# Performance work log

Measured on AMD Instinct MI355X. Metric: run time of the kernel, lower is better.

## Reference

```python
import jax, jax.numpy as jnp
import numpy as np
from jax import lax

K_SIZE = 7
STRIDES = (2, 2, 2, 3)

def causal_conv_block(x, w, b, stride):
    # x: (B, Cin, L); w: (Cout, Cin, K); left-pad K-1 for causality
    xp = jnp.pad(x, ((0, 0), (0, 0), (K_SIZE - 1, 0)))
    y = lax.conv_general_dilated(xp, w, window_strides=(stride,), padding='VALID',
                                 dimension_numbers=('NCH', 'OIH', 'NCH'))
    return jax.nn.elu(y + b[None, :, None])

def vq_indices(z, codebook):
    # z: (B, D, T); codebook: (K, D) -> indices (B, T)
    zt = jnp.transpose(z, (0, 2, 1))                      # (B, T, D)
    d = (jnp.sum(zt * zt, axis=-1, keepdims=True)
         - 2.0 * jnp.einsum('btd,kd->btk', zt, codebook)
         + jnp.sum(codebook * codebook, axis=-1)[None, None, :])  # (B, T, K)
    return jnp.argmin(d, axis=-1)

def setup_inputs() -> dict:
    key = jax.random.key(0)
    ks = jax.random.split(key, 16)
    B, L = 64, 48000
    chans = [1, 16, 32, 64, 64]  # in->out schedule from min(64, 16*2**i)
    inp = {'x': jax.random.normal(ks[0], (B, 1, L), dtype=jnp.float32)}
    for i in range(4):
        cin, cout = chans[i], chans[i + 1]
        scale = 1.0 / np.sqrt(cin * K_SIZE)
        inp[f'w{i}'] = jax.random.normal(ks[1 + 2 * i], (cout, cin, K_SIZE), jnp.float32) * scale
        inp[f'b{i}'] = jax.random.normal(ks[2 + 2 * i], (cout,), jnp.float32) * 0.01
    # pre_quant: 64 -> LATENT_DIM*NUM_CODEBOOKS = 128
    inp['wq'] = jax.random.normal(ks[10], (128, 64, K_SIZE), jnp.float32) * (1.0 / np.sqrt(64 * K_SIZE))
    inp['bq'] = jax.random.normal(ks[11], (128,), jnp.float32) * 0.01
    inp['codebooks'] = jax.random.normal(ks[12], (2, 1024, 64), jnp.float32)  # (num_cb, K, D)
    return inp

def reference(x, w0, b0, w1, b1, w2, b2, w3, b3, wq, bq, codebooks):
    h = x
    for w, b, s in ((w0, b0, STRIDES[0]), (w1, b1, STRIDES[1]),
                    (w2, b2, STRIDES[2]), (w3, b3, STRIDES[3])):
        h = causal_conv_block(h, w, b, s)
    z_e = causal_conv_block(h, wq, bq, 1)           # (B, 128, T)
    z0, z1 = jnp.split(z_e, 2, axis=1)              # chunk along channel dim
    idx0 = vq_indices(z0, codebooks[0])             # (B, T) int
    idx1 = vq_indices(z1, codebooks[1])
    return jnp.stack([idx0, idx1], axis=0)          # (num_cb, B, T)
```

## Files before the change

kernel.cpp:

```cpp
#include <hip/hip_runtime.h>
#include <hip/hip_bf16.h>
#include <cstddef>


using bf16x8 = __attribute__((ext_vector_type(8))) short;
using s16x4  = __attribute__((ext_vector_type(4))) short;
using f32x4  = __attribute__((ext_vector_type(4))) float;

static __device__ __forceinline__ short f2bf(float f) {
    __hip_bfloat16 h = __float2bfloat16(f);
    union { __hip_bfloat16 h; short s; } u; u.h = h;
    return u.s;
}
static __device__ __forceinline__ float bf2f(short s) {
    union { unsigned u; float f; } v;
    v.u = ((unsigned)(unsigned short)s) << 16;
    return v.f;
}
static __device__ __forceinline__ void split3(float v, short& s0, short& s1, short& s2) {
    s0 = f2bf(v);  float r1 = v  - bf2f(s0);
    s1 = f2bf(r1); float r2 = r1 - bf2f(s1);
    s2 = f2bf(r2);
}
static __device__ __forceinline__ float elu(float v) {
    return v > 0.0f ? v : expm1f(v);
}

__global__ __launch_bounds__(256) void conv0_kernel(
    const float* __restrict__ x, const float* __restrict__ w,
    const float* __restrict__ bias, float* __restrict__ H0)
{
    __shared__ float xs[261];
    int tb = blockIdx.x, b = blockIdx.y;
    int t0 = tb * 128;
    int tid = threadIdx.x, lane = tid & 63;
    int wv = __builtin_amdgcn_readfirstlane(tid >> 6);

    const float* xb = x + (size_t)b * 48000;
    int g0 = t0 * 2 - 6;
    for (int i = tid; i < 261; i += 256) {
        int gx = g0 + i;
        xs[i] = (gx >= 0 && gx < 48000) ? xb[gx] : 0.0f;
    }
    __syncthreads();

    int co0 = wv * 4;
    float acc[4][2];
    #pragma unroll
    for (int c = 0; c < 4; ++c) { acc[c][0] = 0.f; acc[c][1] = 0.f; }

    float xw[2][7];
    #pragma unroll
    for (int u = 0; u < 2; ++u)
        #pragma unroll
        for (int k = 0; k < 7; ++k)
            xw[u][k] = xs[(lane + 64 * u) * 2 + k];
    #pragma unroll
    for (int c = 0; c < 4; ++c) {
        const float* wp = w + (size_t)(co0 + c) * 7;
        #pragma unroll
        for (int k = 0; k < 7; ++k) {
            float wk = wp[k];
            acc[c][0] = fmaf(wk, xw[0][k], acc[c][0]);
            acc[c][1] = fmaf(wk, xw[1][k], acc[c][1]);
        }
    }

    #pragma unroll
    for (int u = 0; u < 2; ++u) {
        int t = t0 + lane + 64 * u;
        if (t < 24000) {
            float4 vv;
            vv.x = elu(acc[0][u] + bias[co0 + 0]);
            vv.y = elu(acc[1][u] + bias[co0 + 1]);
            vv.z = elu(acc[2][u] + bias[co0 + 2]);
            vv.w = elu(acc[3][u] + bias[co0 + 3]);
            *(float4*)(H0 + ((size_t)b * 12000 + (t >> 1)) * 32 + (t & 1) * 16 + co0) = vv;
        }
    }
}

template<int CIN, int COUT, int TAPS>
__global__ void wprep3_kernel(const float* __restrict__ w, short* __restrict__ frag)
{
    constexpr int KC = CIN / 32;
    int co = threadIdx.x;
    if (co >= COUT) return;
    int mt = co >> 4, nc = co & 15;
    for (int kc = 0; kc < KC; ++kc)
        for (int k = 0; k < TAPS; ++k)
            #pragma unroll
            for (int lh = 0; lh < 4; ++lh) {
                bf16x8 p0, p1, p2;
                #pragma unroll
                for (int j = 0; j < 8; ++j) {
                    int ci = kc * 32 + lh * 8 + j;
                    float f = w[(size_t)co * CIN * 7 + ci * 7 + k];
                    short a, bb, c; split3(f, a, bb, c);
                    p0[j] = a; p1[j] = bb; p2[j] = c;
                }
                size_t base = ((size_t)(mt * KC + kc) * TAPS + k) * 3;
                int off = (lh * 16 + nc) * 8;
                *(bf16x8*)(frag + (base + 0) * 512 + off) = p0;
                *(bf16x8*)(frag + (base + 1) * 512 + off) = p1;
                *(bf16x8*)(frag + (base + 2) * 512 + off) = p2;
            }
}

template<int CINH, int COUT>
__global__ void wprep3_ps_kernel(const float* __restrict__ w, short* __restrict__ frag)
{
    constexpr int CIN = 2 * CINH;
    constexpr int KC  = CIN / 32;
    int co = threadIdx.x;
    if (co >= COUT) return;
    int mt = co >> 4, nc = co & 15;
    for (int kc = 0; kc < KC; ++kc)
        for (int m = 0; m < 4; ++m)
            #pragma unroll
            for (int lh = 0; lh < 4; ++lh) {
                bf16x8 p0, p1, p2;
                #pragma unroll
                for (int j = 0; j < 8; ++j) {
                    int cp = kc * 32 + lh * 8 + j;
                    float f;
                    if (cp < CINH)  f = w[(size_t)co * CINH * 7 + cp * 7 + 2 * m];
                    else if (m < 3) f = w[(size_t)co * CINH * 7 + (cp - CINH) * 7 + 2 * m + 1];
                    else            f = 0.0f;
                    short a, bb, c; split3(f, a, bb, c);
                    p0[j] = a; p1[j] = bb; p2[j] = c;
                }
                size_t base = ((size_t)(mt * KC + kc) * 4 + m) * 3;
                int off = (lh * 16 + nc) * 8;
                *(bf16x8*)(frag + (base + 0) * 512 + off) = p0;
                *(bf16x8*)(frag + (base + 1) * 512 + off) = p1;
                *(bf16x8*)(frag + (base + 2) * 512 + off) = p2;
            }
}

template<int S, int CIN, int COUT, int NTL, int TAPS, int PAD, int OUTMODE>
__global__ __launch_bounds__(256) void conv_mfma3_kernel(
    const float* __restrict__ Hin, const short* __restrict__ wfrag,
    const float* __restrict__ bias, float* __restrict__ Hout,
    int Lin, int Lout)
{
    constexpr int KC   = CIN / 32;
    constexpr int MT   = COUT / 16;
    constexpr int NT   = NTL * 64;
    constexpr int ROWS = (NT - 1) * S + TAPS;
    constexpr int ROWB = CIN * 2;
    constexpr int NSL  = CIN / 4;
    __shared__ __align__(16) short pl0[ROWS * CIN];
    __shared__ __align__(16) short pl1[ROWS * CIN];
    __shared__ __align__(16) short pl2[ROWS * CIN];

    int nb = blockIdx.x, b = blockIdx.y;
    int t0 = nb * NT;
    int tid = threadIdx.x, lane = tid & 63, wv = tid >> 6;
    int g0 = t0 * S - PAD;

    const float* inb = Hin + (size_t)b * Lin * CIN;
    for (int e = tid; e < ROWS * NSL; e += 256) {
        int rr = e / NSL, sl = e % NSL;
        int g = g0 + rr;
        float4 v = {0.f, 0.f, 0.f, 0.f};
        if (g >= 0 && g < Lin)
            v = *(const float4*)(inb + (size_t)g * CIN + sl * 4);
        int xr = (CIN == 64) ? (rr & 7) : ((rr >> 1) & 3);
        int byte = rr * ROWB + ((((sl >> 1) ^ xr) << 4) | ((sl & 1) << 3));
        s16x4 q0, q1, q2;
        short a0, a1, a2;
        split3(v.x, a0, a1, a2); q0[0] = a0; q1[0] = a1; q2[0] = a2;
        split3(v.y, a0, a1, a2); q0[1] = a0; q1[1] = a1; q2[1] = a2;
        split3(v.z, a0, a1, a2); q0[2] = a0; q1[2] = a1; q2[2] = a2;
        split3(v.w, a0, a1, a2); q0[3] = a0; q1[3] = a1; q2[3] = a2;
        *(s16x4*)((char*)pl0 + byte) = q0;
        *(s16x4*)((char*)pl1 + byte) = q1;
        *(s16x4*)((char*)pl2 + byte) = q2;
    }
    __syncthreads();

    f32x4 acc[NTL][MT];
    #pragma unroll
    for (int n = 0; n < NTL; ++n)
        #pragma unroll
        for (int m = 0; m < MT; ++m) acc[n][m] = (f32x4){0.f, 0.f, 0.f, 0.f};

    int ncol = lane & 15, nq = lane >> 4;

    for (int k = 0; k < TAPS; ++k) {
        #pragma unroll
        for (int kc = 0; kc < KC; ++kc) {
            int colb = (kc * 32 + nq * 8) * 2;
            bf16x8 B0[NTL], B1[NTL], B2[NTL];
            #pragma unroll
            for (int ntl = 0; ntl < NTL; ++ntl) {
                int r  = S * ((wv * NTL + ntl) * 16 + ncol) + k;
                int xr = (CIN == 64) ? (r & 7) : ((r >> 1) & 3);
                int byte = r * ROWB + (colb ^ (xr << 4));
                B0[ntl] = *(const bf16x8*)((char*)pl0 + byte);
                B1[ntl] = *(const bf16x8*)((char*)pl1 + byte);
                B2[ntl] = *(const bf16x8*)((char*)pl2 + byte);
            }
            #pragma unroll
            for (int m = 0; m < MT; ++m) {
                size_t base = ((size_t)(m * KC + kc) * TAPS + k) * 3;
                bf16x8 a0 = *(const bf16x8*)(wfrag + (base + 0) * 512 + lane * 8);
                bf16x8 a1 = *(const bf16x8*)(wfrag + (base + 1) * 512 + lane * 8);
                bf16x8 a2 = *(const bf16x8*)(wfrag + (base + 2) * 512 + lane * 8);
                #pragma unroll
                for (int ntl = 0; ntl < NTL; ++ntl) {
                    f32x4 a = acc[ntl][m];
                    a = __builtin_amdgcn_mfma_f32_16x16x32_bf16(a0, B0[ntl], a, 0, 0, 0);
                    a = __builtin_amdgcn_mfma_f32_16x16x32_bf16(a1, B0[ntl], a, 0, 0, 0);
                    a = __builtin_amdgcn_mfma_f32_16x16x32_bf16(a2, B0[ntl], a, 0, 0, 0);
                    a = __builtin_amdgcn_mfma_f32_16x16x32_bf16(a0, B1[ntl], a, 0, 0, 0);
                    a = __builtin_amdgcn_mfma_f32_16x16x32_bf16(a1, B1[ntl], a, 0, 0, 0);
                    a = __builtin_amdgcn_mfma_f32_16x16x32_bf16(a0, B2[ntl], a, 0, 0, 0);
                    acc[ntl][m] = a;
                }
            }
        }
    }

    #pragma unroll
    for (int ntl = 0; ntl < NTL; ++ntl) {
        int n = t0 + (wv * NTL + ntl) * 16 + ncol;
        if (n < Lout) {
            #pragma unroll
            for (int m = 0; m < MT; ++m) {
                int co0 = m * 16 + nq * 4;
                float4 bb = *(const float4*)(bias + co0);
                float4 vv;
                vv.x = elu(acc[ntl][m][0] + bb.x);
                vv.y = elu(acc[ntl][m][1] + bb.y);
                vv.z = elu(acc[ntl][m][2] + bb.z);
                vv.w = elu(acc[ntl][m][3] + bb.w);
                if constexpr (OUTMODE == 0) {
                    *(float4*)(Hout + ((size_t)b * Lout + n) * COUT + co0) = vv;
                } else if constexpr (OUTMODE == 1) {
                    *(float4*)(Hout + ((size_t)b * (Lout >> 1) + (n >> 1)) * (2 * COUT)
                               + (n & 1) * COUT + co0) = vv;
                } else {
                    Hout[((size_t)b * COUT + co0 + 0) * Lout + n] = vv.x;
                    Hout[((size_t)b * COUT + co0 + 1) * Lout + n] = vv.y;
                    Hout[((size_t)b * COUT + co0 + 2) * Lout + n] = vv.z;
                    Hout[((size_t)b * COUT + co0 + 3) * Lout + n] = vv.w;
                }
            }
        }
    }
}

__global__ __launch_bounds__(256) void vq_prep_kernel(
    const float* __restrict__ cbs, float* __restrict__ cc, short* __restrict__ cbf)
{
    int c = blockIdx.x * 256 + threadIdx.x;
    if (c >= 2048) return;
    int cb = c >> 10, nl = c & 1023;
    const float* row = cbs + (size_t)c * 64;
    float v[64];
    float s = 0.f;
    #pragma unroll
    for (int i = 0; i < 16; ++i) {
        float4 q = ((const float4*)row)[i];
        v[4*i+0] = q.x; v[4*i+1] = q.y; v[4*i+2] = q.z; v[4*i+3] = q.w;
        s += q.x*q.x + q.y*q.y + q.z*q.z + q.w*q.w;
    }
    cc[c] = s;
    int nt = nl >> 4, nc = nl & 15;
    #pragma unroll
    for (int kc = 0; kc < 2; ++kc)
        #pragma unroll
        for (int lh = 0; lh < 4; ++lh) {
            bf16x8 ph, pl;
            #pragma unroll
            for (int j = 0; j < 8; ++j) {
                float f = -2.0f * v[kc*32 + lh*8 + j];
                short h = f2bf(f);
                ph[j] = h;
                pl[j] = f2bf(f - bf2f(h));
            }
            size_t base = ((((size_t)cb*64 + nt)*2 + kc)*2);
            *(bf16x8*)(cbf + ((base + 0)*64 + (lh*16 + nc)) * 8) = ph;
            *(bf16x8*)(cbf + ((base + 1)*64 + (lh*16 + nc)) * 8) = pl;
        }
}

__global__ void zero_cnt_kernel(int* cnt) {
    if (threadIdx.x == 0 && blockIdx.x == 0) { cnt[0] = 0; cnt[1] = 0; }
}

#define VQ_MARGIN 0.04f

__global__ __launch_bounds__(256) void vq_mfma_kernel(
    const float* __restrict__ z, const short* __restrict__ cbf,
    const float* __restrict__ ccg, int* __restrict__ out,
    int* __restrict__ cnt, int* __restrict__ list0, int* __restrict__ list1)
{
    __shared__ short zf[2][8*2*64*8];
    __shared__ short cbc[8*2*2*64*8];

    const int T = 2000;
    int mblk = blockIdx.x;
    int cb   = blockIdx.y;
    int b    = blockIdx.z;
    int t0   = mblk * 128;
    int tid  = threadIdx.x;
    int lane = tid & 63;
    int wv   = tid >> 6;
    int* list = cb ? list1 : list0;

    const float* zb = z + ((size_t)b*128 + (size_t)cb*64) * T;
    for (int e = tid; e < 128 * 8; e += 256) {
        int tl = e & 127;
        int d0 = (e >> 7) * 8;
        int tt = t0 + tl; if (tt > T - 1) tt = T - 1;
        bf16x8 hi, lo;
        #pragma unroll
        for (int jj = 0; jj < 8; ++jj) {
            float v = zb[(size_t)(d0 + jj) * T + tt];
            short h = f2bf(v);
            hi[jj] = h;
            lo[jj] = f2bf(v - bf2f(h));
        }
        int mt = tl >> 4, kc = d0 >> 5;
        int lw = ((d0 & 31) >> 3) * 16 + (tl & 15);
        int idx = ((mt*2 + kc)*64 + lw) * 8;
        *(bf16x8*)&zf[0][idx] = hi;
        *(bf16x8*)&zf[1][idx] = lo;
    }
    __syncthreads();

    bf16x8 ah[2][2], al[2][2];
    #pragma unroll
    for (int mtl = 0; mtl < 2; ++mtl)
        #pragma unroll
        for (int kc = 0; kc < 2; ++kc) {
            int idx = ((((wv*2+mtl)*2 + kc)*64) + lane)*8;
            ah[mtl][kc] = *(const bf16x8*)&zf[0][idx];
            al[mtl][kc] = *(const bf16x8*)&zf[1][idx];
        }

    float best[2][4], second[2][4]; int bidx[2][4];
    #pragma unroll
    for (int m = 0; m < 2; ++m)
        #pragma unroll
        for (int j = 0; j < 4; ++j) { best[m][j] = 3.4e38f; second[m][j] = 3.4e38f; bidx[m][j] = 0; }

    const short* cbase = cbf + (size_t)cb * (64*2*2*64*8);
    const float* ccb   = ccg + cb * 1024;
    int c15 = lane & 15;

    for (int ch = 0; ch < 8; ++ch) {
        __syncthreads();
        {
            const float4* src = (const float4*)(cbase + (size_t)ch * (8*2*2*64*8));
            float4* dst = (float4*)cbc;
            #pragma unroll
            for (int i = 0; i < 8; ++i) dst[tid + 256*i] = src[tid + 256*i];
        }
        __syncthreads();

        #pragma unroll
        for (int ntl = 0; ntl < 8; ++ntl) {
            bf16x8 b0h = *(const bf16x8*)&cbc[(((ntl*2 + 0)*2 + 0)*64 + lane)*8];
            bf16x8 b0l = *(const bf16x8*)&cbc[(((ntl*2 + 0)*2 + 1)*64 + lane)*8];
            bf16x8 b1h = *(const bf16x8*)&cbc[(((ntl*2 + 1)*2 + 0)*64 + lane)*8];
            bf16x8 b1l = *(const bf16x8*)&cbc[(((ntl*2 + 1)*2 + 1)*64 + lane)*8];
            int  code = ch*128 + ntl*16 + c15;
            float ccv = ccb[code];
            #pragma unroll
            for (int mtl = 0; mtl < 2; ++mtl) {
                f32x4 p = {ccv, ccv, ccv, ccv};
                p = __builtin_amdgcn_mfma_f32_16x16x32_bf16(ah[mtl][0], b0h, p, 0, 0, 0);
                p = __builtin_amdgcn_mfma_f32_16x16x32_bf16(al[mtl][0], b0h, p, 0, 0, 0);
                p = __builtin_amdgcn_mfma_f32_16x16x32_bf16(ah[mtl][0], b0l, p, 0, 0, 0);
                p = __builtin_amdgcn_mfma_f32_16x16x32_bf16(ah[mtl][1], b1h, p, 0, 0, 0);
                p = __builtin_amdgcn_mfma_f32_16x16x32_bf16(al[mtl][1], b1h, p, 0, 0, 0);
                p = __builtin_amdgcn_mfma_f32_16x16x32_bf16(ah[mtl][1], b1l, p, 0, 0, 0);
                #pragma unroll
                for (int j = 0; j < 4; ++j) {
                    float s = p[j];
                    bool lt = s < best[mtl][j];
                    second[mtl][j] = __builtin_amdgcn_fmed3f(best[mtl][j], s, second[mtl][j]);
                    best[mtl][j]   = fminf(best[mtl][j], s);
                    bidx[mtl][j]   = lt ? code : bidx[mtl][j];
                }
            }
        }
    }

    #pragma unroll
    for (int m = 0; m < 2; ++m)
        #pragma unroll
        for (int j = 0; j < 4; ++j) {
            float bv = best[m][j], sv = second[m][j]; int bi = bidx[m][j];
            #pragma unroll
            for (int d = 1; d < 16; d <<= 1) {
                float ob = __shfl_xor(bv, d, 64);
                float os = __shfl_xor(sv, d, 64);
                int   oi = __shfl_xor(bi, d, 64);
                float loser = fmaxf(bv, ob);
                sv = fminf(fminf(sv, os), loser);
                bool sw = ob < bv;
                bv = fminf(bv, ob);
                bi = sw ? oi : bi;
            }
            if ((lane & 15) == 0) {
                int t = t0 + (wv*2 + m)*16 + (lane >> 4)*4 + j;
                if (t < T) {
                    out[((size_t)cb*64 + b)*T + t] = bi;
                    if (sv - bv < VQ_MARGIN) {
                        int pos = atomicAdd(&cnt[cb], 1);
                        list[pos] = (b << 11) | t;
                    }
                }
            }
        }
}

__global__ __launch_bounds__(256) void vq_rescore_kernel(
    const float* __restrict__ H3, const float* __restrict__ wq,
    const float* __restrict__ bq, const float* __restrict__ cbs,
    const float* __restrict__ ccg, const int* __restrict__ cnt,
    const int* __restrict__ list0, const int* __restrict__ list1,
    int* __restrict__ out)
{
    const int T = 2000;
    __shared__ float hp[4][2][448];
    __shared__ float zsh[4][2][64];
    int tid = threadIdx.x, lane = tid & 63, wv = tid >> 6;
    int cb = blockIdx.y;
    const int* list = cb ? list1 : list0;
    int count = cnt[cb];
    int gw = blockIdx.x * 4 + wv, nw = gridDim.x * 4;

    const float* cbase = cbs + (size_t)cb * 1024 * 64;
    const float* ccb   = ccg + cb * 1024;
    int d = cb * 64 + lane;
    const float4* wp = (const float4*)(wq + (size_t)d * 448);
    float bqd = bq[d];

    for (int i0 = gw * 2; i0 < count; i0 += nw * 2) {
        int e0 = list[i0];
        int e1 = (i0 + 1 < count) ? list[i0 + 1] : e0;
        int b0 = e0 >> 11, t0 = e0 & 2047;
        int b1 = e1 >> 11, t1 = e1 & 2047;

        size_t base0 = (size_t)b0 * T * 64;
        size_t base1 = (size_t)b1 * T * 64;
        #pragma unroll
        for (int kk = 0; kk < 7; ++kk) {
            int a0 = t0 - 6 + kk, a1 = t1 - 6 + kk;
            hp[wv][0][lane * 7 + kk] = (a0 >= 0) ? H3[base0 + (size_t)a0 * 64 + lane] : 0.0f;
            hp[wv][1][lane * 7 + kk] = (a1 >= 0) ? H3[base1 + (size_t)a1 * 64 + lane] : 0.0f;
        }

        float p00=0.f,p01=0.f,p02=0.f,p03=0.f, p10=0.f,p11=0.f,p12=0.f,p13=0.f;
        #pragma unroll 8
        for (int q = 0; q < 112; ++q) {
            float4 w4 = wp[q];
            float4 h0 = *(const float4*)&hp[wv][0][4 * q];
            float4 h1 = *(const float4*)&hp[wv][1][4 * q];
            p00 = fmaf(w4.x, h0.x, p00); p01 = fmaf(w4.y, h0.y, p01);
            p02 = fmaf(w4.z, h0.z, p02); p03 = fmaf(w4.w, h0.w, p03);
            p10 = fmaf(w4.x, h1.x, p10); p11 = fmaf(w4.y, h1.y, p11);
            p12 = fmaf(w4.z, h1.z, p12); p13 = fmaf(w4.w, h1.w, p13);
        }
        float z0 = (p00 + p01) + (p02 + p03) + bqd; z0 = z0 > 0.f ? z0 : expm1f(z0);
        float z1 = (p10 + p11) + (p12 + p13) + bqd; z1 = z1 > 0.f ? z1 : expm1f(z1);
        zsh[wv][0][lane] = z0;
        zsh[wv][1][lane] = z1;

        float bv0 = 3.4e38f, bv1 = 3.4e38f; int bi0 = 0, bi1 = 0;
        for (int ii = 0; ii < 16; ++ii) {
            int code = ii * 64 + lane;
            const float4* cp = (const float4*)(cbase + (size_t)code * 64);
            float d00=0.f,d01=0.f,d02=0.f,d03=0.f, d10=0.f,d11=0.f,d12=0.f,d13=0.f;
            #pragma unroll
            for (int q = 0; q < 16; ++q) {
                float4 cv = cp[q];
                float4 za = *(const float4*)&zsh[wv][0][4 * q];
                float4 zc = *(const float4*)&zsh[wv][1][4 * q];
                d00 = fmaf(za.x, cv.x, d00); d01 = fmaf(za.y, cv.y, d01);
                d02 = fmaf(za.z, cv.z, d02); d03 = fmaf(za.w, cv.w, d03);
                d10 = fmaf(zc.x, cv.x, d10); d11 = fmaf(zc.y, cv.y, d11);
                d12 = fmaf(zc.z, cv.z, d12); d13 = fmaf(zc.w, cv.w, d13);
            }
            float cc0 = ccb[code];
            float s0 = fmaf(-2.0f, (d00 + d01) + (d02 + d03), cc0);
            float s1 = fmaf(-2.0f, (d10 + d11) + (d12 + d13), cc0);
            if (s0 < bv0) { bv0 = s0; bi0 = code; }
            if (s1 < bv1) { bv1 = s1; bi1 = code; }
        }
        #pragma unroll
        for (int dd = 1; dd < 64; dd <<= 1) {
            float ov0 = __shfl_xor(bv0, dd, 64); int oi0 = __shfl_xor(bi0, dd, 64);
            if (ov0 < bv0 || (ov0 == bv0 && oi0 < bi0)) { bv0 = ov0; bi0 = oi0; }
            float ov1 = __shfl_xor(bv1, dd, 64); int oi1 = __shfl_xor(bi1, dd, 64);
            if (ov1 < bv1 || (ov1 == bv1 && oi1 < bi1)) { bv1 = ov1; bi1 = oi1; }
        }
        if (lane == 0) {
            out[((size_t)cb * 64 + b0) * T + t0] = bi0;
            out[((size_t)cb * 64 + b1) * T + t1] = bi1;
        }
    }
}

extern "C" void kernel_launch(void* const* d_in, const int* in_sizes, int n_in,
                              void* d_out, int out_size, void* d_ws, size_t ws_size,
                              hipStream_t stream)
{
    const float* x   = (const float*)d_in[0];
    const float* w0  = (const float*)d_in[1];
    const float* b0  = (const float*)d_in[2];
    const float* w1  = (const float*)d_in[3];
    const float* b1  = (const float*)d_in[4];
    const float* w2  = (const float*)d_in[5];
    const float* b2  = (const float*)d_in[6];
    const float* w3  = (const float*)d_in[7];
    const float* b3  = (const float*)d_in[8];
    const float* wq  = (const float*)d_in[9];
    const float* bq  = (const float*)d_in[10];
    const float* cbs = (const float*)d_in[11];
    int* out = (int*)d_out;

    char* r1 = (char*)d_ws;
    char* r2 = r1 + 98304000;
    float* H0 = (float*)r1;
    float* H1 = (float*)r2;
    float* H2 = (float*)r1;
    float* H3 = (float*)r2;
    float* z  = (float*)(r2 + 32768000);

    short* wf1 = (short*)d_out;
    short* wf2 = wf1 + 12288;
    short* wf3 = wf1 + 61440;
    short* wf4 = wf1 + 147456;

    short* cbf   = (short*)r1;
    float* cc    = (float*)(r1 + 524288);
    int*   cnt   = (int*)(r1 + 540000);
    int*   list0 = (int*)(r1 + 1000000);
    int*   list1 = (int*)(r1 + 2100000);

    wprep3_ps_kernel<16, 32><<<1, 32, 0, stream>>>(w1, wf1);
    wprep3_ps_kernel<32, 64><<<1, 64, 0, stream>>>(w2, wf2);
    wprep3_kernel<64, 64, 7><<<1, 64, 0, stream>>>(w3, wf3);
    wprep3_kernel<64, 128, 7><<<1, 128, 0, stream>>>(wq, wf4);

    conv0_kernel<<<dim3(188, 64), 256, 0, stream>>>(x, w0, b0, H0);
    conv_mfma3_kernel<1, 32, 32, 2, 4, 3, 1><<<dim3(94, 64), 256, 0, stream>>>(
        H0, wf1, b1, H1, 12000, 12000);
    conv_mfma3_kernel<1, 64, 64, 2, 4, 3, 0><<<dim3(47, 64), 256, 0, stream>>>(
        H1, wf2, b2, H2, 6000, 6000);
    conv_mfma3_kernel<3, 64, 64, 1, 7, 6, 0><<<dim3(32, 64), 256, 0, stream>>>(
        H2, wf3, b3, H3, 6000, 2000);

    vq_prep_kernel<<<8, 256, 0, stream>>>(cbs, cc, cbf);
    zero_cnt_kernel<<<1, 64, 0, stream>>>(cnt);

    conv_mfma3_kernel<1, 64, 128, 2, 7, 6, 2><<<dim3(16, 64), 256, 0, stream>>>(
        H3, wf4, bq, z, 2000, 2000);

    vq_mfma_kernel<<<dim3(16, 2, 64), 256, 0, stream>>>(z, cbf, cc, out, cnt, list0, list1);
    vq_rescore_kernel<<<dim3(512, 2), 256, 0, stream>>>(H3, wq, bq, cbs, cc, cnt, list0, list1, out);
}
```

Baseline: 726.9 us.

## Prefetch next codebook chunk into registers and alias shared buffers in VQ kernel

Changes the VQ MFMA kernel to load the next codebook chunk from global memory into registers while the current chunk is being processed, so the global fetch overlaps compute. The z fragment buffers and the codebook staging buffer now alias one shared array, reducing LDS per block so more blocks may fit per CU. It also raises wave priority around the MFMA sequence. The cost is higher register pressure from holding the prefetched data, which may lower occupancy.

After: 763.8 us. +5.1%, slower.

```diff
diff --git a/kernel.cpp b/kernel.cpp
--- a/kernel.cpp
+++ b/kernel.cpp
@@ -298,8 +298,10 @@
     const float* __restrict__ ccg, int* __restrict__ out,
     int* __restrict__ cnt, int* __restrict__ list0, int* __restrict__ list1)
 {
-    __shared__ short zf[2][8*2*64*8];
-    __shared__ short cbc[8*2*2*64*8];
+    __shared__ __align__(16) short sbuf[16384];
+    short* zf0 = sbuf;
+    short* zf1 = sbuf + 8192;
+    short* cbc = sbuf;
 
     const int T = 2000;
     int mblk = blockIdx.x;
@@ -327,8 +329,8 @@
         int mt = tl >> 4, kc = d0 >> 5;
         int lw = ((d0 & 31) >> 3) * 16 + (tl & 15);
         int idx = ((mt*2 + kc)*64 + lw) * 8;
-        *(bf16x8*)&zf[0][idx] = hi;
-        *(bf16x8*)&zf[1][idx] = lo;
+        *(bf16x8*)&zf0[idx] = hi;
+        *(bf16x8*)&zf1[idx] = lo;
     }
     __syncthreads();
 
@@ -338,8 +340,8 @@
         #pragma unroll
         for (int kc = 0; kc < 2; ++kc) {
             int idx = ((((wv*2+mtl)*2 + kc)*64) + lane)*8;
-            ah[mtl][kc] = *(const bf16x8*)&zf[0][idx];
-            al[mtl][kc] = *(const bf16x8*)&zf[1][idx];
+            ah[mtl][kc] = *(const bf16x8*)&zf0[idx];
+            al[mtl][kc] = *(const bf16x8*)&zf1[idx];
         }
 
     float best[2][4], second[2][4]; int bidx[2][4];
@@ -352,15 +354,26 @@
     const float* ccb   = ccg + cb * 1024;
     int c15 = lane & 15;
 
+    float4 pre[8];
+    {
+        const float4* src = (const float4*)cbase;
+        #pragma unroll
+        for (int i = 0; i < 8; ++i) pre[i] = src[tid + 256*i];
+    }
+
     for (int ch = 0; ch < 8; ++ch) {
         __syncthreads();
         {
-            const float4* src = (const float4*)(cbase + (size_t)ch * (8*2*2*64*8));
             float4* dst = (float4*)cbc;
             #pragma unroll
-            for (int i = 0; i < 8; ++i) dst[tid + 256*i] = src[tid + 256*i];
+            for (int i = 0; i < 8; ++i) dst[tid + 256*i] = pre[i];
         }
         __syncthreads();
+        if (ch < 7) {
+            const float4* src = (const float4*)(cbase + (size_t)(ch + 1) * (8*2*2*64*8));
+            #pragma unroll
+            for (int i = 0; i < 8; ++i) pre[i] = src[tid + 256*i];
+        }
 
         #pragma unroll
         for (int ntl = 0; ntl < 8; ++ntl) {
@@ -373,12 +386,14 @@
             #pragma unroll
             for (int mtl = 0; mtl < 2; ++mtl) {
                 f32x4 p = {ccv, ccv, ccv, ccv};
+                __builtin_amdgcn_s_setprio(1);
                 p = __builtin_amdgcn_mfma_f32_16x16x32_bf16(ah[mtl][0], b0h, p, 0, 0, 0);
                 p = __builtin_amdgcn_mfma_f32_16x16x32_bf16(al[mtl][0], b0h, p, 0, 0, 0);
                 p = __builtin_amdgcn_mfma_f32_16x16x32_bf16(ah[mtl][0], b0l, p, 0, 0, 0);
                 p = __builtin_amdgcn_mfma_f32_16x16x32_bf16(ah[mtl][1], b1h, p, 0, 0, 0);
                 p = __builtin_amdgcn_mfma_f32_16x16x32_bf16(al[mtl][1], b1h, p, 0, 0, 0);
                 p = __builtin_amdgcn_mfma_f32_16x16x32_bf16(ah[mtl][1], b1l, p, 0, 0, 0);
+                __builtin_amdgcn_s_setprio(0);
                 #pragma unroll
                 for (int j = 0; j < 4; ++j) {
                     float s = p[j];
```
